# Optimization experiments

Hardware: AMD Instinct MI355X
Metric: run time of the kernel (lower is better)

Reference implementation:

```python
import math
import jax, jax.numpy as jnp
import numpy as np

B, T, C, H = 2, 2048, 1024, 16
HD = C // H

def gelu_tanh(x):
    # 0.5*x*(1+tanh(sqrt(2/pi)*(x+0.044715*x^3)))
    c = math.sqrt(2.0 / math.pi)
    return 0.5 * x * (1.0 + jnp.tanh(c * (x + 0.044715 * x * x * x)))

def layernorm(x, g, b, eps=1e-5):
    mu = jnp.mean(x, axis=-1, keepdims=True)
    var = jnp.var(x, axis=-1, keepdims=True)
    return (x - mu) * jax.lax.rsqrt(var + eps) * g + b

def setup_inputs() -> dict:
    key = jax.random.key(0)
    ks = jax.random.split(key, 6)
    s = 0.02
    return {
        "x": jax.random.normal(ks[0], (B, T, C), jnp.float32),
        "ln1_g": jnp.ones((C,), jnp.float32),
        "ln1_b": jnp.zeros((C,), jnp.float32),
        "W_qkv": jax.random.normal(ks[1], (C, 3 * C), jnp.float32) * s,
        "b_qkv": jnp.zeros((3 * C,), jnp.float32),
        "W_out": jax.random.normal(ks[2], (C, C), jnp.float32) * s,
        "b_out": jnp.zeros((C,), jnp.float32),
        "ln2_g": jnp.ones((C,), jnp.float32),
        "ln2_b": jnp.zeros((C,), jnp.float32),
        "W_fc1": jax.random.normal(ks[3], (C, 4 * C), jnp.float32) * s,
        "b_fc1": jnp.zeros((4 * C,), jnp.float32),
        "W_fc2": jax.random.normal(ks[4], (4 * C, C), jnp.float32) * s,
        "b_fc2": jnp.zeros((C,), jnp.float32),
    }

def reference(x, ln1_g, ln1_b, W_qkv, b_qkv, W_out, b_out,
              ln2_g, ln2_b, W_fc1, b_fc1, W_fc2, b_fc2):
    # pre-LN causal self-attention
    h = layernorm(x, ln1_g, ln1_b)
    qkv = h @ W_qkv + b_qkv                      # [B,T,3C]
    q, k, v = jnp.split(qkv, 3, axis=-1)
    q = q.reshape(B, T, H, HD).transpose(0, 2, 1, 3)  # [B,H,T,HD]
    k = k.reshape(B, T, H, HD).transpose(0, 2, 1, 3)
    v = v.reshape(B, T, H, HD).transpose(0, 2, 1, 3)
    scores = jnp.einsum("bhqd,bhkd->bhqk", q, k) * (1.0 / math.sqrt(HD))
    causal = jnp.tril(jnp.ones((T, T), bool))
    scores = jnp.where(causal, scores, jnp.float32(-jnp.inf))
    att = jax.nn.softmax(scores, axis=-1)
    out = jnp.einsum("bhqk,bhkd->bhqd", att, v)  # [B,H,T,HD]
    out = out.transpose(0, 2, 1, 3).reshape(B, T, C)
    out = out @ W_out + b_out
    temp = x + out
    # GELU MLP
    h2 = layernorm(temp, ln2_g, ln2_b)
    ff = gelu_tanh(h2 @ W_fc1 + b_fc1) @ W_fc2 + b_fc2
    return temp + ff
```

## Files before the change

### kernel.cpp

```cpp
#include <hip/hip_runtime.h>
#include <stdint.h>

#define Bb 2
#define Tt 2048
#define Cc 1024
#define Hh 16
#define HD 64
#define Mm (Bb*Tt)

typedef __bf16 bf16x8 __attribute__((ext_vector_type(8)));
typedef float  f32x4  __attribute__((ext_vector_type(4)));

#define DEV static __device__ __forceinline__

DEV float asfloat_(uint32_t u){ union{uint32_t u; float f;} x; x.u=u; return x.f; }
DEV uint32_t asuint_(float f){ union{float f; uint32_t u;} x; x.f=f; return x.u; }
DEV unsigned short f2bf(float f){
  uint32_t u = asuint_(f);
  uint32_t r = (u + 0x7fffu + ((u>>16)&1u)) >> 16;
  return (unsigned short)r;
}
DEV float gelu_(float x){
  float x3 = x*x*x;
  float t  = 0.7978845608028654f * (x + 0.044715f*x3);
  float e  = __expf(2.0f*t);
  float th = 1.0f - 2.0f/(e + 1.0f);
  return 0.5f * x * (1.0f + th);
}

#define GLL(gsrc, ldst) __builtin_amdgcn_global_load_lds( \
    (const __attribute__((address_space(1))) void*)(gsrc), \
    (__attribute__((address_space(3))) void*)(ldst), 16, 0, 0)

__global__ void wcvt_kernel(const float* __restrict__ W, unsigned short* __restrict__ WT,
                            int K, int N) {
  __shared__ float tile[32][33];
  int tx = threadIdx.x & 31, ty = threadIdx.x >> 5;
  int kb = blockIdx.x * 32, nb = blockIdx.y * 32;
  #pragma unroll
  for (int r = 0; r < 32; r += 8)
    tile[ty + r][tx] = W[(size_t)(kb + ty + r) * N + nb + tx];
  __syncthreads();
  #pragma unroll
  for (int r = 0; r < 32; r += 8)
    WT[(size_t)(nb + ty + r) * K + kb + tx] = f2bf(tile[tx][ty + r]);
}

__global__ void ln_kernel(const float* __restrict__ X, const float* __restrict__ g,
                          const float* __restrict__ bb, unsigned short* __restrict__ O) {
  int row = blockIdx.x, t = threadIdx.x;
  const float4* xr = (const float4*)(X + (size_t)row * Cc);
  float4 v = xr[t];
  float s = v.x + v.y + v.z + v.w;
  float q = v.x*v.x + v.y*v.y + v.z*v.z + v.w*v.w;
  #pragma unroll
  for (int o = 32; o > 0; o >>= 1) { s += __shfl_xor(s, o); q += __shfl_xor(q, o); }
  __shared__ float ss[4], sq[4];
  int w = t >> 6;
  if ((t & 63) == 0) { ss[w] = s; sq[w] = q; }
  __syncthreads();
  s = ss[0] + ss[1] + ss[2] + ss[3];
  q = sq[0] + sq[1] + sq[2] + sq[3];
  float mu  = s * (1.0f/Cc);
  float var = q * (1.0f/Cc) - mu*mu;
  float rstd = rsqrtf(var + 1e-5f);
  float4 gv = ((const float4*)g)[t], bv = ((const float4*)bb)[t];
  ushort4 o4;
  o4.x = f2bf((v.x-mu)*rstd*gv.x + bv.x);
  o4.y = f2bf((v.y-mu)*rstd*gv.y + bv.y);
  o4.z = f2bf((v.z-mu)*rstd*gv.z + bv.z);
  o4.w = f2bf((v.w-mu)*rstd*gv.w + bv.w);
  ((ushort4*)(O + (size_t)row * Cc))[t] = o4;
}

template<int MODE>
__launch_bounds__(512, 4)
__global__ void gemm_kernel(const unsigned short* __restrict__ A,
                            const unsigned short* __restrict__ BT,
                            const float* __restrict__ bias,
                            const float* __restrict__ res,
                            void* __restrict__ Cout,
                            int N, int K) {
  __shared__ unsigned short As[128*64];
  __shared__ unsigned short Bs[128*64];
  int tid  = threadIdx.x;
  int lane = tid & 63, w = tid >> 6;
  int wr = w >> 2, wc = w & 3;
  int g = lane >> 4, ql = lane & 15;
  int bm = blockIdx.x, bn = blockIdx.y;

  f32x4 acc[4][2];
  #pragma unroll
  for (int m = 0; m < 4; ++m)
    #pragma unroll
    for (int n = 0; n < 2; ++n) acc[m][n] = (f32x4){0.f,0.f,0.f,0.f};

  int r  = tid >> 3;
  int cc = tid & 7;
  int sc = (cc ^ (r & 7)) * 8;
  const unsigned short* Ag = A  + (size_t)(bm*128 + r) * K + sc;
  const unsigned short* Bg = BT + (size_t)(bn*128 + r) * K + sc;
  int sw = (ql & 7) << 3;
  int nk = K >> 6;

  for (int kt = 0; kt < nk; ++kt) {
    if (kt) __syncthreads();
    const unsigned short* ag = Ag + kt*64;
    const unsigned short* bg = Bg + kt*64;
    GLL(ag,                  As + w*512);
    GLL(ag + (size_t)64*K,   As + 4096 + w*512);
    GLL(bg,                  Bs + w*512);
    GLL(bg + (size_t)64*K,   Bs + 4096 + w*512);
    __syncthreads();

    #pragma unroll
    for (int kk = 0; kk < 2; ++kk) {
      int col = (kk*32 + g*8) ^ sw;
      bf16x8 af[4], bf2[2];
      #pragma unroll
      for (int m = 0; m < 4; ++m)
        af[m] = *(const bf16x8*)(As + (wr*64 + m*16 + ql)*64 + col);
      #pragma unroll
      for (int n = 0; n < 2; ++n)
        bf2[n] = *(const bf16x8*)(Bs + (wc*32 + n*16 + ql)*64 + col);
      #pragma unroll
      for (int m = 0; m < 4; ++m)
        #pragma unroll
        for (int n = 0; n < 2; ++n)
          acc[m][n] = __builtin_amdgcn_mfma_f32_16x16x32_bf16(af[m], bf2[n], acc[m][n], 0, 0, 0);
    }
  }

  int r0 = bm*128 + wr*64;
  int c0 = bn*128 + wc*32;
  int lr = g * 4;
  #pragma unroll
  for (int m = 0; m < 4; ++m) {
    #pragma unroll
    for (int n = 0; n < 2; ++n) {
      int col = c0 + n*16 + ql;
      float bv = bias[col];
      #pragma unroll
      for (int i = 0; i < 4; ++i) {
        int row = r0 + m*16 + lr + i;
        float v = acc[m][n][i] + bv;
        if (MODE == 2) v = gelu_(v);
        ((unsigned short*)Cout)[(size_t)row * N + col] = f2bf(v);
      }
    }
  }
}

__launch_bounds__(1024, 2)
__global__ void gemm_skrf_kernel(const unsigned short* __restrict__ A,
                                 const unsigned short* __restrict__ BT,
                                 const float* __restrict__ bias,
                                 const float* __restrict__ res,
                                 float* __restrict__ Cout,
                                 int N, int K) {
  __shared__ __align__(16) unsigned short SMEM[32768];
  int tid  = threadIdx.x;
  int lane = tid & 63, w = tid >> 6;
  int wg = w >> 3, w8 = w & 7;
  int wr = w8 >> 2, wc = w8 & 3;
  int g = lane >> 4, ql = lane & 15;
  int bm = blockIdx.x, bn = blockIdx.y;

  unsigned short* AsH = SMEM + wg*8192;
  unsigned short* BsH = SMEM + 16384 + wg*8192;

  f32x4 acc[4][2];
  #pragma unroll
  for (int m = 0; m < 4; ++m)
    #pragma unroll
    for (int n = 0; n < 2; ++n) acc[m][n] = (f32x4){0.f,0.f,0.f,0.f};

  int tid_h = tid & 511;
  int r  = tid_h >> 3;
  int cc = tid_h & 7;
  int sc = (cc ^ (r & 7)) * 8;
  int kbase = wg * (K >> 1);
  const unsigned short* Ag = A  + (size_t)(bm*128 + r) * K + kbase + sc;
  const unsigned short* Bg = BT + (size_t)(bn*128 + r) * K + kbase + sc;
  int sw = (ql & 7) << 3;
  int nk = K >> 7;

  for (int kt = 0; kt < nk; ++kt) {
    if (kt) __syncthreads();
    const unsigned short* ag = Ag + kt*64;
    const unsigned short* bg = Bg + kt*64;
    GLL(ag,                  AsH + w8*512);
    GLL(ag + (size_t)64*K,   AsH + 4096 + w8*512);
    GLL(bg,                  BsH + w8*512);
    GLL(bg + (size_t)64*K,   BsH + 4096 + w8*512);
    __syncthreads();

    #pragma unroll
    for (int kk = 0; kk < 2; ++kk) {
      int col = (kk*32 + g*8) ^ sw;
      bf16x8 af[4], bf2[2];
      #pragma unroll
      for (int m = 0; m < 4; ++m)
        af[m] = *(const bf16x8*)(AsH + (wr*64 + m*16 + ql)*64 + col);
      #pragma unroll
      for (int n = 0; n < 2; ++n)
        bf2[n] = *(const bf16x8*)(BsH + (wc*32 + n*16 + ql)*64 + col);
      #pragma unroll
      for (int m = 0; m < 4; ++m)
        #pragma unroll
        for (int n = 0; n < 2; ++n)
          acc[m][n] = __builtin_amdgcn_mfma_f32_16x16x32_bf16(af[m], bf2[n], acc[m][n], 0, 0, 0);
    }
  }

  __syncthreads();
  float* ex = (float*)SMEM;
  int eb = (w8*64 + lane) * 32;
  if (wg == 1) {
    #pragma unroll
    for (int m = 0; m < 4; ++m)
      #pragma unroll
      for (int n = 0; n < 2; ++n) {
        int c = m*2 + n;
        *(f32x4*)&ex[eb + ((c ^ (lane & 7)) << 2)] = acc[m][n];
      }
  }
  __syncthreads();
  if (wg == 0) {
    #pragma unroll
    for (int m = 0; m < 4; ++m)
      #pragma unroll
      for (int n = 0; n < 2; ++n) {
        int c = m*2 + n;
        f32x4 o = *(const f32x4*)&ex[eb + ((c ^ (lane & 7)) << 2)];
        acc[m][n][0] += o[0]; acc[m][n][1] += o[1];
        acc[m][n][2] += o[2]; acc[m][n][3] += o[3];
      }
    int r0 = bm*128 + wr*64;
    int c0 = bn*128 + wc*32;
    int lr = g * 4;
    #pragma unroll
    for (int m = 0; m < 4; ++m) {
      #pragma unroll
      for (int n = 0; n < 2; ++n) {
        int col = c0 + n*16 + ql;
        float bv = bias[col];
        #pragma unroll
        for (int i = 0; i < 4; ++i) {
          int row = r0 + m*16 + lr + i;
          Cout[(size_t)row * N + col] = acc[m][n][i] + bv + res[(size_t)row * N + col];
        }
      }
    }
  }
}

__global__ void vtr_kernel(const unsigned short* __restrict__ qkv,
                           unsigned short* __restrict__ vtb) {
  __shared__ unsigned short Tl[64][72];
  int tid = threadIdx.x;
  int bh = blockIdx.x, tc = blockIdx.y;
  int b = bh >> 4, h = bh & 15;
  int r = tid >> 2, c0 = (tid & 3) * 16;
  const unsigned short* src = qkv + (size_t)(b*Tt + tc*64 + r)*3072 + 2048 + h*64 + c0;
  *(int4*)&Tl[r][c0]     = *(const int4*)(src);
  *(int4*)&Tl[r][c0 + 8] = *(const int4*)(src + 8);
  __syncthreads();
  int d = tid >> 2, k0 = (tid & 3) * 16;
  ushort4 o[4];
  #pragma unroll
  for (int jj = 0; jj < 4; ++jj) {
    o[jj].x = Tl[k0 + jj*4 + 0][d];
    o[jj].y = Tl[k0 + jj*4 + 1][d];
    o[jj].z = Tl[k0 + jj*4 + 2][d];
    o[jj].w = Tl[k0 + jj*4 + 3][d];
  }
  unsigned short* dst = vtb + ((size_t)(bh*64 + d))*2048 + tc*64 + k0;
  *(int4*)(dst)     = *(int4*)&o[0];
  *(int4*)(dst + 8) = *(int4*)&o[2];
}

__global__ __launch_bounds__(512, 4)
void attn_kernel(const unsigned short* __restrict__ qkv,
                 const unsigned short* __restrict__ vtb,
                 unsigned short* __restrict__ att) {
  __shared__ __align__(16) char smem[36864];
  int tid  = threadIdx.x;
  int lane = tid & 63, w = tid >> 6;
  int g = lane >> 4, ql = lane & 15;

  int bid = blockIdx.x;
  int bh = bid & 31;
  int jj = bid >> 5;
  int j  = (jj < 8) ? (2*jj) : (31 - 2*jj);
  int b = bh >> 4, h = bh & 15;
  int Q0 = j * 128;
  int qbase = Q0 + w * 16;
  char* Pb = smem + 16384 + w * 2560;

  const unsigned short* qrow = qkv + (size_t)(b*Tt + qbase + ql) * 3072 + h*64;
  bf16x8 qf0 = *(const bf16x8*)(qrow + g*8);
  bf16x8 qf1 = *(const bf16x8*)(qrow + 32 + g*8);

  f32x4 O[4];
  #pragma unroll
  for (int d = 0; d < 4; ++d) O[d] = (f32x4){0.f,0.f,0.f,0.f};
  float mrun = -1e30f, lrun = 0.f;

  int nt = Q0/64 + 2;

  int srow = tid >> 3;
  int scol = (tid & 7) * 8;
  int wr_off = srow*128 + ((scol*2) ^ ((srow & 7) << 4));
  const unsigned short* Kg = qkv + (size_t)(b*Tt + srow)*3072 + 1024 + h*64 + scol;
  const unsigned short* Vg = vtb + ((size_t)(bh*64 + srow))*2048 + scol;

  int4 kreg = *(const int4*)(Kg);
  int4 vreg = *(const int4*)(Vg);

  for (int t0 = 0; t0 < nt; ++t0) {
    __syncthreads();
    *(int4*)(smem + wr_off)        = kreg;
    *(int4*)(smem + 8192 + wr_off) = vreg;
    __syncthreads();
    if (t0 + 1 < nt) {
      kreg = *(const int4*)(Kg + (size_t)(t0+1)*64*3072);
      vreg = *(const int4*)(Vg + (t0+1)*64);
    }
    if (t0*64 > qbase + 15) continue;

    bool full = (t0*64 + 63) <= qbase;
    float ps[16];
    #pragma unroll
    for (int s = 0; s < 4; ++s) {
      int krow = s*16 + ql;
      int kb0 = krow*128 + (( g*16      ) ^ ((krow&7)<<4));
      int kb1 = krow*128 + (( g*16 + 64 ) ^ ((krow&7)<<4));
      bf16x8 kf0 = *(const bf16x8*)(smem + kb0);
      bf16x8 kf1 = *(const bf16x8*)(smem + kb1);
      f32x4 a = (f32x4){0.f,0.f,0.f,0.f};
      a = __builtin_amdgcn_mfma_f32_16x16x32_bf16(kf0, qf0, a, 0, 0, 0);
      a = __builtin_amdgcn_mfma_f32_16x16x32_bf16(kf1, qf1, a, 0, 0, 0);
      #pragma unroll
      for (int i = 0; i < 4; ++i) ps[s*4+i] = a[i] * 0.125f;
    }
    if (!full) {
      #pragma unroll
      for (int s = 0; s < 4; ++s)
        #pragma unroll
        for (int i = 0; i < 4; ++i)
          if (t0*64 + s*16 + g*4 + i > qbase + ql) ps[s*4+i] = -1e30f;
    }
    float tm = ps[0];
    #pragma unroll
    for (int i = 1; i < 16; ++i) tm = fmaxf(tm, ps[i]);
    tm = fmaxf(tm, __shfl_xor(tm, 16));
    tm = fmaxf(tm, __shfl_xor(tm, 32));
    float mnew = fmaxf(mrun, tm);
    float corr = __expf(mrun - mnew);
    float tsum = 0.f;
    #pragma unroll
    for (int s = 0; s < 4; ++s) {
      float e0 = __expf(ps[s*4+0] - mnew);
      float e1 = __expf(ps[s*4+1] - mnew);
      float e2 = __expf(ps[s*4+2] - mnew);
      float e3 = __expf(ps[s*4+3] - mnew);
      tsum += (e0 + e1) + (e2 + e3);
      ushort4 pk;
      pk.x = f2bf(e0); pk.y = f2bf(e1); pk.z = f2bf(e2); pk.w = f2bf(e3);
      *(ushort4*)(Pb + ql*160 + s*32 + g*8) = pk;
    }
    tsum += __shfl_xor(tsum, 16);
    tsum += __shfl_xor(tsum, 32);
    lrun = lrun * corr + tsum;
    mrun = mnew;

    float c0 = __shfl(corr, g*4 + 0);
    float c1 = __shfl(corr, g*4 + 1);
    float c2 = __shfl(corr, g*4 + 2);
    float c3 = __shfl(corr, g*4 + 3);
    #pragma unroll
    for (int d = 0; d < 4; ++d) {
      O[d][0] *= c0; O[d][1] *= c1; O[d][2] *= c2; O[d][3] *= c3;
    }
    #pragma unroll
    for (int kk = 0; kk < 2; ++kk) {
      bf16x8 pf = *(const bf16x8*)(Pb + ql*160 + kk*64 + g*16);
      #pragma unroll
      for (int d = 0; d < 4; ++d) {
        int drow = d*16 + ql;
        int vb = drow*128 + ((kk*64 + g*16) ^ ((drow&7)<<4));
        bf16x8 vf = *(const bf16x8*)(smem + 8192 + vb);
        O[d] = __builtin_amdgcn_mfma_f32_16x16x32_bf16(pf, vf, O[d], 0, 0, 0);
      }
    }
  }

  float l0 = __shfl(lrun, g*4 + 0);
  float l1 = __shfl(lrun, g*4 + 1);
  float l2 = __shfl(lrun, g*4 + 2);
  float l3 = __shfl(lrun, g*4 + 3);
  #pragma unroll
  for (int d = 0; d < 4; ++d) {
    size_t base = (size_t)(b*Tt + qbase)*Cc + h*64 + d*16 + ql;
    att[base + (size_t)(g*4+0)*Cc] = f2bf(O[d][0] / l0);
    att[base + (size_t)(g*4+1)*Cc] = f2bf(O[d][1] / l1);
    att[base + (size_t)(g*4+2)*Cc] = f2bf(O[d][2] / l2);
    att[base + (size_t)(g*4+3)*Cc] = f2bf(O[d][3] / l3);
  }
}

extern "C" void kernel_launch(void* const* d_in, const int* in_sizes, int n_in,
                              void* d_out, int out_size, void* d_ws, size_t ws_size,
                              hipStream_t stream) {
  const float* x    = (const float*)d_in[0];
  const float* ln1g = (const float*)d_in[1];
  const float* ln1b = (const float*)d_in[2];
  const float* Wqkv = (const float*)d_in[3];
  const float* bqkv = (const float*)d_in[4];
  const float* Wout = (const float*)d_in[5];
  const float* bout = (const float*)d_in[6];
  const float* ln2g = (const float*)d_in[7];
  const float* ln2b = (const float*)d_in[8];
  const float* Wfc1 = (const float*)d_in[9];
  const float* bfc1 = (const float*)d_in[10];
  const float* Wfc2 = (const float*)d_in[11];
  const float* bfc2 = (const float*)d_in[12];

  char* ws = (char*)d_ws;
  unsigned short* wqkvT = (unsigned short*)(ws);
  unsigned short* woutT = (unsigned short*)(ws + (6u<<20));
  unsigned short* wfc1T = (unsigned short*)(ws + (8u<<20));
  unsigned short* wfc2T = (unsigned short*)(ws + (16u<<20));
  unsigned short* vtb   = (unsigned short*)(ws + (24u<<20));
  float*          temp  = (float*)(ws + (24u<<20));
  unsigned short* hbuf  = (unsigned short*)(ws + (40u<<20));
  unsigned short* qkvb  = (unsigned short*)(ws + (48u<<20));
  unsigned short* attb  = (unsigned short*)(ws + (72u<<20));
  unsigned short* a1b   = (unsigned short*)(ws + (48u<<20));

  dim3 b256(256), b512(512), b1024(1024);
  wcvt_kernel<<<dim3(1024/32, 3072/32), b256, 0, stream>>>(Wqkv, wqkvT, 1024, 3072);
  wcvt_kernel<<<dim3(1024/32, 1024/32), b256, 0, stream>>>(Wout, woutT, 1024, 1024);
  wcvt_kernel<<<dim3(1024/32, 4096/32), b256, 0, stream>>>(Wfc1, wfc1T, 1024, 4096);
  wcvt_kernel<<<dim3(4096/32, 1024/32), b256, 0, stream>>>(Wfc2, wfc2T, 4096, 1024);

  ln_kernel<<<Mm, b256, 0, stream>>>(x, ln1g, ln1b, hbuf);
  gemm_kernel<0><<<dim3(Mm/128, 3072/128), b512, 0, stream>>>(hbuf, wqkvT, bqkv, nullptr, qkvb, 3072, 1024);
  vtr_kernel<<<dim3(32, 32), b256, 0, stream>>>(qkvb, vtb);
  attn_kernel<<<dim3(512), 512, 0, stream>>>(qkvb, vtb, attb);
  gemm_skrf_kernel<<<dim3(Mm/128, 1024/128), b1024, 0, stream>>>(attb, woutT, bout, x, temp, 1024, 1024);
  ln_kernel<<<Mm, b256, 0, stream>>>(temp, ln2g, ln2b, hbuf);
  gemm_kernel<2><<<dim3(Mm/128, 4096/128), b512, 0, stream>>>(hbuf, wfc1T, bfc1, nullptr, a1b, 4096, 1024);
  gemm_skrf_kernel<<<dim3(Mm/128, 1024/128), b1024, 0, stream>>>(a1b, wfc2T, bfc2, temp, (float*)d_out, 1024, 4096);
}
```

Before: 356.1 us.

## Double-buffer LDS tiles in GEMM kernels to overlap global loads with MFMA

Both GEMM kernels now keep two LDS buffers and issue the direct-to-LDS global loads for the next K tile before computing on the current one, with a single barrier per iteration. This is meant to hide global memory latency behind MFMA work. It doubles LDS usage (64 KB per block for the 512-thread kernel, 128 KB for the split-K kernel), which can cut occupancy. Correctness relies on the barrier waiting for the asynchronous LDS loads to complete.

After: 323.4 us. 1.1x faster.

```diff
diff --git a/kernel.cpp b/kernel.cpp
--- a/kernel.cpp
+++ b/kernel.cpp
@@ -81,8 +81,8 @@
                             const float* __restrict__ res,
                             void* __restrict__ Cout,
                             int N, int K) {
-  __shared__ unsigned short As[128*64];
-  __shared__ unsigned short Bs[128*64];
+  __shared__ unsigned short As[2][128*64];
+  __shared__ unsigned short Bs[2][128*64];
   int tid  = threadIdx.x;
   int lane = tid & 63, w = tid >> 6;
   int wr = w >> 2, wc = w & 3;
@@ -103,32 +103,42 @@
   int sw = (ql & 7) << 3;
   int nk = K >> 6;
 
+  GLL(Ag,                 As[0] + w*512);
+  GLL(Ag + (size_t)64*K,  As[0] + 4096 + w*512);
+  GLL(Bg,                 Bs[0] + w*512);
+  GLL(Bg + (size_t)64*K,  Bs[0] + 4096 + w*512);
+  __syncthreads();
+
+  int cur = 0;
   for (int kt = 0; kt < nk; ++kt) {
-    if (kt) __syncthreads();
-    const unsigned short* ag = Ag + kt*64;
-    const unsigned short* bg = Bg + kt*64;
-    GLL(ag,                  As + w*512);
-    GLL(ag + (size_t)64*K,   As + 4096 + w*512);
-    GLL(bg,                  Bs + w*512);
-    GLL(bg + (size_t)64*K,   Bs + 4096 + w*512);
-    __syncthreads();
-
+    if (kt + 1 < nk) {
+      const unsigned short* ag = Ag + (kt+1)*64;
+      const unsigned short* bg = Bg + (kt+1)*64;
+      GLL(ag,                 As[cur^1] + w*512);
+      GLL(ag + (size_t)64*K,  As[cur^1] + 4096 + w*512);
+      GLL(bg,                 Bs[cur^1] + w*512);
+      GLL(bg + (size_t)64*K,  Bs[cur^1] + 4096 + w*512);
+    }
+    const unsigned short* Asc = As[cur];
+    const unsigned short* Bsc = Bs[cur];
     #pragma unroll
     for (int kk = 0; kk < 2; ++kk) {
       int col = (kk*32 + g*8) ^ sw;
       bf16x8 af[4], bf2[2];
       #pragma unroll
       for (int m = 0; m < 4; ++m)
-        af[m] = *(const bf16x8*)(As + (wr*64 + m*16 + ql)*64 + col);
+        af[m] = *(const bf16x8*)(Asc + (wr*64 + m*16 + ql)*64 + col);
       #pragma unroll
       for (int n = 0; n < 2; ++n)
-        bf2[n] = *(const bf16x8*)(Bs + (wc*32 + n*16 + ql)*64 + col);
+        bf2[n] = *(const bf16x8*)(Bsc + (wc*32 + n*16 + ql)*64 + col);
       #pragma unroll
       for (int m = 0; m < 4; ++m)
         #pragma unroll
         for (int n = 0; n < 2; ++n)
           acc[m][n] = __builtin_amdgcn_mfma_f32_16x16x32_bf16(af[m], bf2[n], acc[m][n], 0, 0, 0);
     }
+    __syncthreads();
+    cur ^= 1;
   }
 
   int r0 = bm*128 + wr*64;
@@ -158,16 +168,13 @@
                                  const float* __restrict__ res,
                                  float* __restrict__ Cout,
                                  int N, int K) {
-  __shared__ __align__(16) unsigned short SMEM[32768];
+  __shared__ __align__(16) unsigned short SMEM[2][32768];
   int tid  = threadIdx.x;
   int lane = tid & 63, w = tid >> 6;
   int wg = w >> 3, w8 = w & 7;
   int wr = w8 >> 2, wc = w8 & 3;
   int g = lane >> 4, ql = lane & 15;
   int bm = blockIdx.x, bn = blockIdx.y;
-
-  unsigned short* AsH = SMEM + wg*8192;
-  unsigned short* BsH = SMEM + 16384 + wg*8192;
 
   f32x4 acc[4][2];
   #pragma unroll
@@ -185,16 +192,25 @@
   int sw = (ql & 7) << 3;
   int nk = K >> 7;
 
+  GLL(Ag,                 SMEM[0] + wg*8192 + w8*512);
+  GLL(Ag + (size_t)64*K,  SMEM[0] + wg*8192 + 4096 + w8*512);
+  GLL(Bg,                 SMEM[0] + 16384 + wg*8192 + w8*512);
+  GLL(Bg + (size_t)64*K,  SMEM[0] + 16384 + wg*8192 + 4096 + w8*512);
+  __syncthreads();
+
+  int cur = 0;
   for (int kt = 0; kt < nk; ++kt) {
-    if (kt) __syncthreads();
-    const unsigned short* ag = Ag + kt*64;
-    const unsigned short* bg = Bg + kt*64;
-    GLL(ag,                  AsH + w8*512);
-    GLL(ag + (size_t)64*K,   AsH + 4096 + w8*512);
-    GLL(bg,                  BsH + w8*512);
-    GLL(bg + (size_t)64*K,   BsH + 4096 + w8*512);
-    __syncthreads();
-
+    if (kt + 1 < nk) {
+      const unsigned short* ag = Ag + (kt+1)*64;
+      const unsigned short* bg = Bg + (kt+1)*64;
+      unsigned short* nb = SMEM[cur^1];
+      GLL(ag,                 nb + wg*8192 + w8*512);
+      GLL(ag + (size_t)64*K,  nb + wg*8192 + 4096 + w8*512);
+      GLL(bg,                 nb + 16384 + wg*8192 + w8*512);
+      GLL(bg + (size_t)64*K,  nb + 16384 + wg*8192 + 4096 + w8*512);
+    }
+    const unsigned short* AsH = SMEM[cur] + wg*8192;
+    const unsigned short* BsH = SMEM[cur] + 16384 + wg*8192;
     #pragma unroll
     for (int kk = 0; kk < 2; ++kk) {
       int col = (kk*32 + g*8) ^ sw;
@@ -211,10 +227,11 @@
         for (int n = 0; n < 2; ++n)
           acc[m][n] = __builtin_amdgcn_mfma_f32_16x16x32_bf16(af[m], bf2[n], acc[m][n], 0, 0, 0);
     }
-  }
-
-  __syncthreads();
-  float* ex = (float*)SMEM;
+    __syncthreads();
+    cur ^= 1;
+  }
+
+  float* ex = (float*)SMEM[0];
   int eb = (w8*64 + lane) * 32;
   if (wg == 1) {
     #pragma unroll
```
